# Performance work log

Measured on AMD Instinct MI355X. Metric: run time of the kernel, lower is better.

## Reference

```python
import jax, jax.numpy as jnp
import numpy as np

B, F, D = 2048, 64, 512   # batch, num_fields, embedding_dim
A = 512                   # attention_dim (== embedding_dim -> W_res is None)
H = 8                     # num_heads
HD = A // H               # head_dim


def setup_inputs() -> dict:
    key = jax.random.key(0)
    ks = jax.random.split(key, 11)
    s = 0.02
    return {
        "query": jax.random.normal(ks[0], (B, F, D), jnp.float32),
        "key":   jax.random.normal(ks[1], (B, F, D), jnp.float32),
        "value": jax.random.normal(ks[2], (B, F, D), jnp.float32),
        "Wq":  jax.random.normal(ks[3], (D, A), jnp.float32) * s,
        "bq":  jnp.zeros((A,), jnp.float32),
        "Wk":  jax.random.normal(ks[4], (D, A), jnp.float32) * s,
        "bk":  jnp.zeros((A,), jnp.float32),
        "Wv":  jax.random.normal(ks[5], (D, A), jnp.float32) * s,
        "bv":  jnp.zeros((A,), jnp.float32),
        "Wk2": jax.random.normal(ks[6], (D, A), jnp.float32) * s,
        "bk2": jnp.zeros((A,), jnp.float32),
    }


def reference(query, key, value, Wq, bq, Wk, bk, Wv, bv, Wk2, bk2):
    b, f, _ = query.shape
    heads = lambda x: x.reshape(b, f, H, HD)  # split(head_dim)+cat(dim=0) == head reshape
    Q  = heads(query @ Wq  + bq)   # [b,f,h,d]
    K  = heads(key   @ Wk  + bk)
    V  = heads(value @ Wv  + bv)
    K2 = heads(key   @ Wk2 + bk2)
    # mean-centering over the field axis (dim=1 in torch)
    Qc = Q - Q.mean(axis=1, keepdims=True)
    Kc = K - K.mean(axis=1, keepdims=True)
    mu_K2 = K2.mean(axis=1)  # [b,h,d]
    # pairwise term: softmax over keys (use_scale=False)
    pairwise = jax.nn.softmax(jnp.einsum('bqhd,bkhd->bhqk', Qc, Kc), axis=-1)
    # unary term: bmm(mu_K2, Kc^T) -> [bh,1,f]; torch softmaxes dim=1 (the size-1
    # query axis), which is faithful-but-degenerate (evaluates to ones). Preserve it.
    unary = jnp.einsum('bhd,bkhd->bhk', mu_K2, Kc)[:, :, None, :]  # [b,h,1,f]
    unary = jax.nn.softmax(unary, axis=2)
    out = jnp.einsum('bhqk,bkhd->bqhd', pairwise + unary, V).reshape(b, f, H * HD)
    out = out + query  # use_residual=True, W_res is None since D == A
    return jax.nn.relu(out)
```

## Files before the change

kernel.cpp:

```cpp
#include <hip/hip_runtime.h>

#define BB 2048
#define FF 64
#define DD 512
#define AA 512
#define HH 8
#define HD 64
#define MM (BB*FF)

typedef unsigned short ushort_t;
typedef __bf16 bf16x8_t __attribute__((ext_vector_type(8)));
typedef float f32x4_t __attribute__((ext_vector_type(4)));

__device__ __forceinline__ ushort_t f2b(float f){
  unsigned x = __float_as_uint(f);
  return (ushort_t)((x + 0x7fffu + ((x>>16)&1u)) >> 16);
}
__device__ __forceinline__ float b2f(ushort_t u){
  return __uint_as_float(((unsigned)u)<<16);
}
__device__ __forceinline__ bf16x8_t ld_frag(const ushort_t* p){
  union { uint4 u; bf16x8_t b; } t;
  t.u = *(const uint4*)p;
  return t.b;
}

__global__ __launch_bounds__(256) void prep_w(const float* __restrict__ Wq,
                                              const float* __restrict__ Wk,
                                              const float* __restrict__ Wv,
                                              ushort_t* __restrict__ WT){
  const int mat = blockIdx.z;
  const float* W = (mat==0) ? Wq : ((mat==1) ? Wk : Wv);
  ushort_t* o = WT + (size_t)mat*DD*AA;
  __shared__ float tile[32][33];
  const int t = threadIdx.x;
  const int k0 = blockIdx.x*32, n0 = blockIdx.y*32;
#pragma unroll
  for(int it=0; it<4; ++it){
    int idx = t + it*256; int r = idx>>5, c = idx&31;
    tile[r][c] = W[(size_t)(k0+r)*AA + n0 + c];
  }
  __syncthreads();
#pragma unroll
  for(int it=0; it<4; ++it){
    int idx = t + it*256; int r = idx>>5, c = idx&31;
    o[(size_t)(n0+r)*DD + k0 + c] = f2b(tile[c][r]);
  }
}

__global__ __launch_bounds__(256) void gemm_qkv(const float* __restrict__ q,
                                                const float* __restrict__ k,
                                                const float* __restrict__ v,
                                                const ushort_t* __restrict__ WTall,
                                                const float* __restrict__ bv,
                                                ushort_t* __restrict__ Call){
  const int bx = blockIdx.x;
  const int mat = bx >> 2;
  const int nb  = bx & 3;
  const float* Ain = (mat==0) ? q : ((mat==1) ? k : v);
  const ushort_t* WT = WTall + (size_t)mat*DD*AA;
  ushort_t* Cout = Call + (size_t)mat*MM*AA;
  const int m0 = blockIdx.y * 128;
  const int n0 = nb * 128;

  __shared__ __align__(16) ushort_t As[128][40];
  __shared__ __align__(16) ushort_t Bs[128][40];

  const int t = threadIdx.x;
  const int wid = t >> 6, lane = t & 63;
  const int wm = wid >> 1, wn = wid & 1;
  const int lm = lane & 15, lk = lane >> 4;

  f32x4_t acc[4][4];
#pragma unroll
  for(int a=0;a<4;++a)
#pragma unroll
    for(int bq=0;bq<4;++bq) acc[a][bq] = (f32x4_t){0.f,0.f,0.f,0.f};

  for(int k0=0; k0<DD; k0+=32){
    __syncthreads();
#pragma unroll
    for(int it=0; it<4; ++it){
      int idx = t + it*256;
      int r = idx >> 3;
      int c4 = (idx & 7) * 4;
      const float4 f = *(const float4*)(Ain + (size_t)(m0+r)*DD + k0 + c4);
      uint2 u;
      u.x = (unsigned)f2b(f.x) | ((unsigned)f2b(f.y) << 16);
      u.y = (unsigned)f2b(f.z) | ((unsigned)f2b(f.w) << 16);
      *(uint2*)&As[r][c4] = u;
    }
#pragma unroll
    for(int it=0; it<2; ++it){
      int idx = t + it*256;
      int r = idx >> 2;
      int c8 = (idx & 3) * 8;
      uint4 w = *(const uint4*)(WT + (size_t)(n0+r)*DD + k0 + c8);
      *(uint4*)&Bs[r][c8] = w;
    }
    __syncthreads();

    bf16x8_t af[4], bfv[4];
#pragma unroll
    for(int mt=0; mt<4; ++mt) af[mt]  = ld_frag(&As[wm*64 + mt*16 + lm][lk*8]);
#pragma unroll
    for(int nt=0; nt<4; ++nt) bfv[nt] = ld_frag(&Bs[wn*64 + nt*16 + lm][lk*8]);
#pragma unroll
    for(int mt=0; mt<4; ++mt)
#pragma unroll
      for(int nt=0; nt<4; ++nt)
        acc[mt][nt] = __builtin_amdgcn_mfma_f32_16x16x32_bf16(af[mt], bfv[nt], acc[mt][nt], 0, 0, 0);
  }

  if(mat == 2){
    const int bb = (m0 >> 6) + wm;
#pragma unroll
    for(int nt=0; nt<4; ++nt){
      const int col = n0 + wn*64 + nt*16 + lm;
      const float bias = bv[col];
      ushort_t* vrow = Cout + ((size_t)bb*AA + col)*FF;
#pragma unroll
      for(int mt=0; mt<4; ++mt){
        const int f0 = mt*16 + lk*4;
        uint2 u;
        u.x = (unsigned)f2b(acc[mt][nt][0] + bias) | ((unsigned)f2b(acc[mt][nt][1] + bias) << 16);
        u.y = (unsigned)f2b(acc[mt][nt][2] + bias) | ((unsigned)f2b(acc[mt][nt][3] + bias) << 16);
        *(uint2*)(vrow + f0) = u;
      }
    }
  } else {
#pragma unroll
    for(int nt=0; nt<4; ++nt){
      const int col = n0 + wn*64 + nt*16 + lm;
#pragma unroll
      for(int mt=0; mt<4; ++mt){
#pragma unroll
        for(int reg=0; reg<4; ++reg){
          const int row = m0 + wm*64 + mt*16 + lk*4 + reg;
          Cout[(size_t)row*AA + col] = f2b(acc[mt][nt][reg]);
        }
      }
    }
  }
}

__global__ __launch_bounds__(256) void attn(const ushort_t* __restrict__ Qws,
                                            const ushort_t* __restrict__ Kws,
                                            const ushort_t* __restrict__ Vt,
                                            const float* __restrict__ query,
                                            float* __restrict__ out){
  const int b = blockIdx.x;
  const int t = threadIdx.x;
  __shared__ float mu[DD];
  __shared__ float vsum[DD];
  __shared__ float uu[HH][FF];
  __shared__ __align__(16) ushort_t P[4][64][72];

  const ushort_t* Qb = Qws + (size_t)b*FF*AA;
  const ushort_t* Kb = Kws + (size_t)b*FF*AA;
  const ushort_t* Vb = Vt  + (size_t)b*AA*FF;

  {
    float s0=0.f, s1=0.f;
#pragma unroll 8
    for(int f=0; f<FF; ++f){
      const ushort_t* qr = Qb + f*AA;
      s0 += b2f(qr[t]);     s1 += b2f(qr[t+256]);
    }
    mu[t]     = s0 * (1.f/64.f);
    mu[t+256] = s1 * (1.f/64.f);
  }
  {
#pragma unroll
    for(int it=0; it<2; ++it){
      const int d = t + it*256;
      const ushort_t* vr = Vb + (size_t)d*FF;
      float a = 0.f;
#pragma unroll
      for(int c=0; c<8; ++c){
        union { uint4 u; ushort_t s[8]; } w;
        w.u = *(const uint4*)(vr + c*8);
#pragma unroll
        for(int j=0; j<8; ++j) a += b2f(w.s[j]);
      }
      vsum[d] = a;
    }
  }
  __syncthreads();

#pragma unroll
  for(int it=0; it<2; ++it){
    int idx = t + it*256;
    int h = idx >> 6, kk = idx & 63;
    const ushort_t* Kr = Kb + kk*AA + h*HD;
    float a = 0.f;
#pragma unroll
    for(int c=0; c<8; ++c){
      union { uint4 u; ushort_t s[8]; } w;
      w.u = *(const uint4*)(Kr + c*8);
#pragma unroll
      for(int j=0; j<8; ++j) a += mu[h*HD + c*8 + j] * b2f(w.s[j]);
    }
    uu[h][kk] = a;
  }
  __syncthreads();

  const int wave = t >> 6, lane = t & 63;
  const int lm = lane & 15, lk = lane >> 4;

  for(int hh=0; hh<2; ++hh){
    const int h = wave*2 + hh;

    f32x4_t acc[4][4];
#pragma unroll
    for(int a=0;a<4;++a)
#pragma unroll
      for(int bq=0;bq<4;++bq) acc[a][bq] = (f32x4_t){0.f,0.f,0.f,0.f};
#pragma unroll
    for(int ks=0; ks<2; ++ks){
      bf16x8_t af[4], bfv[4];
#pragma unroll
      for(int mt=0; mt<4; ++mt)
        af[mt]  = ld_frag(Qb + (size_t)(mt*16+lm)*AA + h*HD + ks*32 + lk*8);
#pragma unroll
      for(int nt=0; nt<4; ++nt)
        bfv[nt] = ld_frag(Kb + (size_t)(nt*16+lm)*AA + h*HD + ks*32 + lk*8);
#pragma unroll
      for(int mt=0; mt<4; ++mt)
#pragma unroll
        for(int nt=0; nt<4; ++nt)
          acc[mt][nt] = __builtin_amdgcn_mfma_f32_16x16x32_bf16(af[mt], bfv[nt], acc[mt][nt], 0, 0, 0);
    }

    float uval[4];
#pragma unroll
    for(int nt=0; nt<4; ++nt) uval[nt] = uu[h][nt*16 + lm];

#pragma unroll
    for(int mt=0; mt<4; ++mt){
#pragma unroll
      for(int reg=0; reg<4; ++reg){
        float x0 = acc[mt][0][reg] - uval[0];
        float x1 = acc[mt][1][reg] - uval[1];
        float x2 = acc[mt][2][reg] - uval[2];
        float x3 = acc[mt][3][reg] - uval[3];
        float m = fmaxf(fmaxf(x0,x1), fmaxf(x2,x3));
        m = fmaxf(m, __shfl_xor(m, 1));
        m = fmaxf(m, __shfl_xor(m, 2));
        m = fmaxf(m, __shfl_xor(m, 4));
        m = fmaxf(m, __shfl_xor(m, 8));
        float e0 = __expf(x0-m), e1 = __expf(x1-m), e2 = __expf(x2-m), e3 = __expf(x3-m);
        float s = e0+e1+e2+e3;
        s += __shfl_xor(s, 1);
        s += __shfl_xor(s, 2);
        s += __shfl_xor(s, 4);
        s += __shfl_xor(s, 8);
        const float inv = 1.f / s;
        const int row = mt*16 + lk*4 + reg;
        P[wave][row][0*16 + lm] = f2b(e0*inv);
        P[wave][row][1*16 + lm] = f2b(e1*inv);
        P[wave][row][2*16 + lm] = f2b(e2*inv);
        P[wave][row][3*16 + lm] = f2b(e3*inv);
      }
    }

    f32x4_t acc2[4][4];
#pragma unroll
    for(int a=0;a<4;++a)
#pragma unroll
      for(int bq=0;bq<4;++bq) acc2[a][bq] = (f32x4_t){0.f,0.f,0.f,0.f};
#pragma unroll
    for(int ks=0; ks<2; ++ks){
      bf16x8_t pf[4], vf[4];
#pragma unroll
      for(int mt=0; mt<4; ++mt)
        pf[mt] = ld_frag(&P[wave][mt*16 + lm][ks*32 + lk*8]);
#pragma unroll
      for(int nt=0; nt<4; ++nt)
        vf[nt] = ld_frag(Vb + (size_t)(h*HD + nt*16 + lm)*FF + ks*32 + lk*8);
#pragma unroll
      for(int mt=0; mt<4; ++mt)
#pragma unroll
        for(int nt=0; nt<4; ++nt)
          acc2[mt][nt] = __builtin_amdgcn_mfma_f32_16x16x32_bf16(pf[mt], vf[nt], acc2[mt][nt], 0, 0, 0);
    }

#pragma unroll
    for(int mt=0; mt<4; ++mt){
#pragma unroll
      for(int nt=0; nt<4; ++nt){
        const int dd = h*HD + nt*16 + lm;
#pragma unroll
        for(int reg=0; reg<4; ++reg){
          const int qrow = mt*16 + lk*4 + reg;
          const size_t gi = ((size_t)b*FF + qrow)*DD + dd;
          float val = acc2[mt][nt][reg] + vsum[dd] + query[gi];
          out[gi] = fmaxf(val, 0.f);
        }
      }
    }
  }
}

extern "C" void kernel_launch(void* const* d_in, const int* in_sizes, int n_in,
                              void* d_out, int out_size, void* d_ws, size_t ws_size,
                              hipStream_t stream){
  const float* query = (const float*)d_in[0];
  const float* key   = (const float*)d_in[1];
  const float* value = (const float*)d_in[2];
  const float* Wq    = (const float*)d_in[3];
  const float* Wk    = (const float*)d_in[5];
  const float* Wv    = (const float*)d_in[7];
  const float* bv    = (const float*)d_in[8];

  ushort_t* WT  = (ushort_t*)d_ws;
  ushort_t* QKV = (ushort_t*)((char*)d_ws + (size_t)(1<<21));
  float* out = (float*)d_out;

  prep_w<<<dim3(16,16,3), 256, 0, stream>>>(Wq, Wk, Wv, WT);
  gemm_qkv<<<dim3(12,1024), 256, 0, stream>>>(query, key, value, WT, bv, QKV);
  attn<<<2048, 256, 0, stream>>>(QKV,
                                 QKV + (size_t)MM*AA,
                                 QKV + 2*(size_t)MM*AA,
                                 query, out);
}
```

Measured before the change: 1.353 ms.

## Use direct global-to-LDS async loads with XOR swizzle and XCD-aware block mapping

After: 1.201 ms. 1.13x faster.

```diff
diff --git a/kernel.cpp b/kernel.cpp
--- a/kernel.cpp
+++ b/kernel.cpp
@@ -1,4 +1,5 @@
 #include <hip/hip_runtime.h>
+#include <stdint.h>
 
 #define BB 2048
 #define FF 64
@@ -23,6 +24,13 @@
   union { uint4 u; bf16x8_t b; } t;
   t.u = *(const uint4*)p;
   return t.b;
+}
+
+__device__ __forceinline__ void async16(void* lds, const void* g){
+  __builtin_amdgcn_global_load_lds(
+      (const __attribute__((address_space(1))) uint32_t*)(uintptr_t)g,
+      (__attribute__((address_space(3))) uint32_t*)(uint32_t)(uintptr_t)lds,
+      16, 0, 0);
 }
 
 __global__ __launch_bounds__(256) void prep_w(const float* __restrict__ Wq,
@@ -54,17 +62,23 @@
                                                 const ushort_t* __restrict__ WTall,
                                                 const float* __restrict__ bv,
                                                 ushort_t* __restrict__ Call){
-  const int bx = blockIdx.x;
-  const int mat = bx >> 2;
-  const int nb  = bx & 3;
+  const int bid = blockIdx.x;
+  const int xcd = bid & 7;
+  const int j   = bid >> 3;
+  const int mat = j / 512;
+  const int r0  = j % 512;
+  const int mb  = xcd*128 + (r0 >> 2);
+  const int nb  = r0 & 3;
+  const int m0  = mb * 128;
+  const int n0  = nb * 128;
+
   const float* Ain = (mat==0) ? q : ((mat==1) ? k : v);
   const ushort_t* WT = WTall + (size_t)mat*DD*AA;
   ushort_t* Cout = Call + (size_t)mat*MM*AA;
-  const int m0 = blockIdx.y * 128;
-  const int n0 = nb * 128;
-
-  __shared__ __align__(16) ushort_t As[128][40];
-  __shared__ __align__(16) ushort_t Bs[128][40];
+
+  __shared__ __align__(16) unsigned char smem[49152];
+  unsigned char* As = smem;
+  unsigned char* Bs = smem + 32768;
 
   const int t = threadIdx.x;
   const int wid = t >> 6, lane = t & 63;
@@ -77,39 +91,53 @@
 #pragma unroll
     for(int bq=0;bq<4;++bq) acc[a][bq] = (f32x4_t){0.f,0.f,0.f,0.f};
 
-  for(int k0=0; k0<DD; k0+=32){
+  const char* Ab = (const char*)(Ain + (size_t)m0*DD);
+  const char* Bb = (const char*)(WT + (size_t)n0*DD);
+
+  for(int k0=0; k0<DD; k0+=64){
     __syncthreads();
 #pragma unroll
-    for(int it=0; it<4; ++it){
-      int idx = t + it*256;
-      int r = idx >> 3;
-      int c4 = (idx & 7) * 4;
-      const float4 f = *(const float4*)(Ain + (size_t)(m0+r)*DD + k0 + c4);
-      uint2 u;
-      u.x = (unsigned)f2b(f.x) | ((unsigned)f2b(f.y) << 16);
-      u.y = (unsigned)f2b(f.z) | ((unsigned)f2b(f.w) << 16);
-      *(uint2*)&As[r][c4] = u;
-    }
-#pragma unroll
-    for(int it=0; it<2; ++it){
-      int idx = t + it*256;
-      int r = idx >> 2;
-      int c8 = (idx & 3) * 8;
-      uint4 w = *(const uint4*)(WT + (size_t)(n0+r)*DD + k0 + c8);
-      *(uint4*)&Bs[r][c8] = w;
+    for(int i=0;i<8;++i){
+      const int L  = i*256 + t;
+      const int rr = L >> 4, ss = L & 15;
+      const int ch = ss ^ (rr & 15);
+      async16(As + L*16, Ab + (size_t)rr*2048 + (size_t)k0*4 + ch*16);
+    }
+#pragma unroll
+    for(int i=0;i<4;++i){
+      const int L  = i*256 + t;
+      const int rr = L >> 3, ss = L & 7;
+      const int ch = ss ^ (rr & 7);
+      async16(Bs + L*16, Bb + (size_t)rr*1024 + (size_t)k0*2 + ch*16);
     }
     __syncthreads();
 
-    bf16x8_t af[4], bfv[4];
-#pragma unroll
-    for(int mt=0; mt<4; ++mt) af[mt]  = ld_frag(&As[wm*64 + mt*16 + lm][lk*8]);
-#pragma unroll
-    for(int nt=0; nt<4; ++nt) bfv[nt] = ld_frag(&Bs[wn*64 + nt*16 + lm][lk*8]);
-#pragma unroll
-    for(int mt=0; mt<4; ++mt)
-#pragma unroll
-      for(int nt=0; nt<4; ++nt)
-        acc[mt][nt] = __builtin_amdgcn_mfma_f32_16x16x32_bf16(af[mt], bfv[nt], acc[mt][nt], 0, 0, 0);
+#pragma unroll
+    for(int kk=0; kk<2; ++kk){
+      bf16x8_t af[4], bfv[4];
+#pragma unroll
+      for(int mt=0; mt<4; ++mt){
+        const int ra = wm*64 + mt*16 + lm;
+        const int c0 = kk*8 + lk*2;
+        const f32x4_t a0 = *(const f32x4_t*)(As + ra*256 + ((c0    ) ^ (ra & 15))*16);
+        const f32x4_t a1 = *(const f32x4_t*)(As + ra*256 + ((c0 + 1) ^ (ra & 15))*16);
+        union { bf16x8_t v; __bf16 e[8]; } u;
+        u.e[0]=(__bf16)a0[0]; u.e[1]=(__bf16)a0[1]; u.e[2]=(__bf16)a0[2]; u.e[3]=(__bf16)a0[3];
+        u.e[4]=(__bf16)a1[0]; u.e[5]=(__bf16)a1[1]; u.e[6]=(__bf16)a1[2]; u.e[7]=(__bf16)a1[3];
+        af[mt] = u.v;
+      }
+#pragma unroll
+      for(int nt=0; nt<4; ++nt){
+        const int rb = wn*64 + nt*16 + lm;
+        const int ch = kk*4 + lk;
+        bfv[nt] = *(const bf16x8_t*)(Bs + rb*128 + ((ch ^ (rb & 7)))*16);
+      }
+#pragma unroll
+      for(int mt=0; mt<4; ++mt)
+#pragma unroll
+        for(int nt=0; nt<4; ++nt)
+          acc[mt][nt] = __builtin_amdgcn_mfma_f32_16x16x32_bf16(af[mt], bfv[nt], acc[mt][nt], 0, 0, 0);
+    }
   }
 
   if(mat == 2){
@@ -318,7 +346,7 @@
   float* out = (float*)d_out;
 
   prep_w<<<dim3(16,16,3), 256, 0, stream>>>(Wq, Wk, Wv, WT);
-  gemm_qkv<<<dim3(12,1024), 256, 0, stream>>>(query, key, value, WT, bv, QKV);
+  gemm_qkv<<<12288, 256, 0, stream>>>(query, key, value, WT, bv, QKV);
   attn<<<2048, 256, 0, stream>>>(QKV,
                                  QKV + (size_t)MM*AA,
                                  QKV + 2*(size_t)MM*AA,
```
